# Optimization experiments

Hardware: AMD Instinct MI355X
Metric: run time of the kernel (lower is better)

## Reference

```python
import jax, jax.numpy as jnp
import numpy as np

B, D, S, F, C, H, OUT = 4, 60, 512, 158, 64, 128, 1
LN_EPS = 1e-5


def setup_inputs() -> dict:
    key = jax.random.key(0)
    ks = jax.random.split(key, 12)
    g = lambda k, shape, s=0.05: jax.random.normal(k, shape, dtype=jnp.float32) * s
    return dict(
        x=jax.random.normal(ks[0], (B, D, S, F), dtype=jnp.float32),
        feature_mask=jax.random.randint(ks[1], (B, D, S), 0, 2).astype(bool),
        wq=g(ks[2], (F, C)), bq=jnp.zeros((C,), jnp.float32),
        wk=g(ks[3], (F, C)), bk=jnp.zeros((C,), jnp.float32),
        wv=g(ks[4], (F, C)), bv=jnp.zeros((C,), jnp.float32),
        ln_g=jnp.ones((F + C,), jnp.float32), ln_b=jnp.zeros((F + C,), jnp.float32),
        w_ih=g(ks[5], (3 * H, F + C)), w_hh=g(ks[6], (3 * H, H)),
        b_ih=jnp.zeros((3 * H,), jnp.float32), b_hh=jnp.zeros((3 * H,), jnp.float32),
        w1=g(ks[7], (H, H // 2)), b1=jnp.zeros((H // 2,), jnp.float32),
        w2=g(ks[8], (H // 2, OUT)), b2=jnp.zeros((OUT,), jnp.float32),
    )


def reference(x, feature_mask, wq, bq, wk, bk, wv, bv, ln_g, ln_b,
              w_ih, w_hh, b_ih, b_hh, w1, b1, w2, b2):
    b, d, s, f = x.shape
    c = wq.shape[1]
    h_dim = w_hh.shape[1]

    # --- market context attention, vectorized over (batch, days) ---
    Q = x @ wq + bq            # (B,D,S,C)
    K = x @ wk + bk
    V = x @ wv + bv
    scores = jnp.einsum('bdsc,bdtc->bdst', Q, K) / jnp.sqrt(jnp.float32(c))
    scores = jnp.where(feature_mask[:, :, None, :], scores, -1e9)  # mask keys
    attn = jax.nn.softmax(scores, axis=-1)
    ctx = jnp.einsum('bdst,bdtc->bdsc', attn, V)       # (B,D,S,C)
    ctx = jnp.where(feature_mask[..., None], ctx, 0.0)  # mask queries
    denom = jnp.maximum(feature_mask.sum(axis=2), 1).astype(x.dtype)  # (B,D)
    market = ctx.sum(axis=2) / denom[..., None]         # (B,D,C)

    # --- concat + layernorm ---
    aug = jnp.concatenate(
        [x, jnp.broadcast_to(market[:, :, None, :], (b, d, s, c))], axis=-1)
    mu = aug.mean(-1, keepdims=True)
    var = aug.var(-1, keepdims=True)
    aug = (aug - mu) / jnp.sqrt(var + LN_EPS) * ln_g + ln_b  # (B,D,S,F+C)

    # --- GRU over days, batch = B*S independent sequences ---
    seq = aug.transpose(1, 0, 2, 3).reshape(d, b * s, f + c)  # (D, N, F+C)
    x_proj = seq @ w_ih.T + b_ih                               # (D, N, 3H)

    def step(h, xp):
        hp = h @ w_hh.T + b_hh
        xr, xz, xn = jnp.split(xp, 3, axis=-1)
        hr, hz, hn = jnp.split(hp, 3, axis=-1)
        r = jax.nn.sigmoid(xr + hr)
        z = jax.nn.sigmoid(xz + hz)
        n = jnp.tanh(xn + r * hn)
        return (1.0 - z) * n + z * h, None

    h0 = jnp.zeros((b * s, h_dim), x.dtype)
    h_last, _ = jax.lax.scan(step, h0, x_proj)  # last-step output
    h_last = h_last.reshape(b, s, h_dim)

    # --- output head (dropout inactive in eval) ---
    hid = jax.nn.relu(h_last @ w1 + b1)
    return hid @ w2 + b2  # (B, S, OUT)
```

## Files before the change

### kernel.cpp

```cpp
#include <hip/hip_runtime.h>
#include <hip/hip_bf16.h>
#include <math.h>

#define BB 4
#define DD 60
#define SS 512
#define FF 158
#define CC 64
#define HH 128
#define FC 222
#define G3 384
#define NN 2048
#define BDN 240

#define L2E  1.44269504f
#define L2E2 2.88539008f
#define QSCALE 0.18033688f

typedef _Float16 f16x8 __attribute__((ext_vector_type(8)));
typedef _Float16 f16x4 __attribute__((ext_vector_type(4)));
typedef float f32x4 __attribute__((ext_vector_type(4)));

__device__ __forceinline__ float exp2_hw(float x){ return __builtin_amdgcn_exp2f(x); }
__device__ __forceinline__ float rcp_hw(float x){ return __builtin_amdgcn_rcpf(x); }

__global__ void prep_kernel(const float* __restrict__ w_ih,
                            const float* __restrict__ wq, const float* __restrict__ wk,
                            const float* __restrict__ w_hh,
                            _Float16* __restrict__ wf16, _Float16* __restrict__ wqk,
                            _Float16* __restrict__ whh16){
    int idx = blockIdx.x*256 + threadIdx.x;
    if (idx < 384*224){
        int n = idx / 224, k = idx % 224;
        float sc = (n < 256) ? L2E : L2E2;
        wf16[idx] = (k < FC) ? (_Float16)(w_ih[n*FC + k] * sc) : (_Float16)0.0f;
    } else if (idx < 384*224 + 128*160){
        int i2 = idx - 384*224;
        int n = i2 / 160, k = i2 % 160;
        float v = 0.0f;
        if (k < FF)
            v = (n < 64) ? wq[k*CC + n] : wk[k*CC + (n-64)];
        wqk[i2] = (_Float16)v;
    } else {
        int i3 = idx - (384*224 + 128*160);
        if (i3 < 384*128){
            int n = i3 / 128;
            float sc = (n < 256) ? L2E : L2E2;
            whh16[i3] = (_Float16)(w_hh[i3] * sc);
        }
    }
}

__global__ __launch_bounds__(256) void qk_kernel(const float* __restrict__ x,
                           const _Float16* __restrict__ wqk,
                           const float* __restrict__ bq, const float* __restrict__ bk,
                           _Float16* __restrict__ Qh, _Float16* __restrict__ Kh){
    __shared__ _Float16 xa[5][64][40];
    int tid  = threadIdx.x;
    int lane = tid & 63, wv = tid >> 6;
    int col  = lane & 15, quad = lane >> 4;
    int row0 = blockIdx.x * 64;

    f16x8 bfr[2][5];
    #pragma unroll
    for (int nt = 0; nt < 2; ++nt){
        int n = wv*32 + nt*16 + col;
        #pragma unroll
        for (int kq = 0; kq < 5; ++kq)
            bfr[nt][kq] = *(const f16x8*)&wqk[n*160 + kq*32 + quad*8];
    }

    if (tid < 128){
        int r = tid >> 1;
        xa[4][r][30 + (tid & 1)] = (_Float16)0.0f;
    }
    {
        const float4* xb4 = (const float4*)(x + (size_t)row0*FF);
        #pragma unroll
        for (int j = 0; j < 10; ++j){
            int i = tid + j*256;
            if (i < 2528){
                float4 v = xb4[i];
                int base = i*4;
                #pragma unroll
                for (int e = 0; e < 4; ++e){
                    int idx = base + e;
                    int r = idx / 158;
                    int k = idx - r*158;
                    xa[k >> 5][r][k & 31] = (_Float16)((&v.x)[e]);
                }
            }
        }
    }
    __syncthreads();

    float bias[2];
    #pragma unroll
    for (int nt = 0; nt < 2; ++nt){
        int n = wv*32 + nt*16 + col;
        bias[nt] = (n < 64) ? bq[n] : bk[n-64];
    }

    #pragma unroll 1
    for (int mt = 0; mt < 4; ++mt){
        f16x8 a[5];
        #pragma unroll
        for (int kq = 0; kq < 5; ++kq)
            a[kq] = *(const f16x8*)&xa[kq][mt*16 + col][quad*8];
        #pragma unroll
        for (int nt = 0; nt < 2; ++nt){
            f32x4 c = {0.0f, 0.0f, 0.0f, 0.0f};
            #pragma unroll
            for (int kq = 0; kq < 5; ++kq)
                c = __builtin_amdgcn_mfma_f32_16x16x32_f16(a[kq], bfr[nt][kq], c, 0, 0, 0);
            int n = wv*32 + nt*16 + col;
            #pragma unroll
            for (int reg = 0; reg < 4; ++reg){
                int row = row0 + mt*16 + quad*4 + reg;
                float val = c[reg] + bias[nt];
                if (n < 64) Qh[(size_t)row*CC + n]      = (_Float16)(val * QSCALE);
                else        Kh[(size_t)row*CC + (n-64)] = (_Float16)val;
            }
        }
    }
}

__global__ __launch_bounds__(512) void attn_kernel(const _Float16* __restrict__ Qh,
                                                   const _Float16* __restrict__ Kh,
                                                   const int* __restrict__ mask,
                                                   const float* __restrict__ x,
                                                   const float* __restrict__ wv,
                                                   const float* __restrict__ bv,
                                                   float* __restrict__ market){
    __shared__ _Float16 kf[2][512][32];
    __shared__ float w_sh[512];
    __shared__ float mk_lds[512];

    int tid  = threadIdx.x;
    int bd   = blockIdx.x;
    int lane = tid & 63, wvw = tid >> 6;
    int col  = lane & 15, quad = lane >> 4;

    const _Float16* qb = Qh + (size_t)(bd*SS)*CC;
    const _Float16* kb = Kh + (size_t)(bd*SS)*CC;

    {
        int t = tid;
        w_sh[t] = 0.0f;
        mk_lds[t] = (mask[bd*SS + t] != 0) ? 1.0f : 0.0f;
    }
    for (int i = tid; i < 4096; i += 512){
        int t = i >> 3, ch = i & 7;
        *(f16x8*)&kf[ch >> 2][t][(ch & 3)*8] = *(const f16x8*)&kb[t*CC + ch*8];
    }

    f16x8 a0[4], a1[4];
    #pragma unroll
    for (int af = 0; af < 4; ++af){
        int row = wvw*64 + af*16 + col;
        a0[af] = *(const f16x8*)&qb[row*CC + quad*8];
        a1[af] = *(const f16x8*)&qb[row*CC + 32 + quad*8];
    }
    __syncthreads();

    float lacc[4][4] = {{0,0,0,0},{0,0,0,0},{0,0,0,0},{0,0,0,0}};
    #pragma unroll 2
    for (int kt = 0; kt < 32; ++kt){
        f16x8 b0 = *(const f16x8*)&kf[0][kt*16 + col][quad*8];
        f16x8 b1 = *(const f16x8*)&kf[1][kt*16 + col][quad*8];
        float mkv = mk_lds[kt*16 + col];
        #pragma unroll
        for (int af = 0; af < 4; ++af){
            f32x4 c = {0.0f, 0.0f, 0.0f, 0.0f};
            c = __builtin_amdgcn_mfma_f32_16x16x32_f16(a0[af], b0, c, 0, 0, 0);
            c = __builtin_amdgcn_mfma_f32_16x16x32_f16(a1[af], b1, c, 0, 0, 0);
            #pragma unroll
            for (int reg = 0; reg < 4; ++reg)
                lacc[af][reg] += exp2_hw(c[reg]) * mkv;
        }
    }
    float crv[4][4];
    #pragma unroll
    for (int af = 0; af < 4; ++af){
        #pragma unroll
        for (int reg = 0; reg < 4; ++reg){
            float l = lacc[af][reg];
            l += __shfl_xor(l, 1, 64);
            l += __shfl_xor(l, 2, 64);
            l += __shfl_xor(l, 4, 64);
            l += __shfl_xor(l, 8, 64);
            int row = wvw*64 + af*16 + quad*4 + reg;
            crv[af][reg] = mk_lds[row] * rcp_hw(l);
        }
    }

    #pragma unroll 2
    for (int kt = 0; kt < 32; ++kt){
        f16x8 b0 = *(const f16x8*)&kf[0][kt*16 + col][quad*8];
        f16x8 b1 = *(const f16x8*)&kf[1][kt*16 + col][quad*8];
        float s = 0.0f;
        #pragma unroll
        for (int af = 0; af < 4; ++af){
            f32x4 c = {0.0f, 0.0f, 0.0f, 0.0f};
            c = __builtin_amdgcn_mfma_f32_16x16x32_f16(a0[af], b0, c, 0, 0, 0);
            c = __builtin_amdgcn_mfma_f32_16x16x32_f16(a1[af], b1, c, 0, 0, 0);
            #pragma unroll
            for (int reg = 0; reg < 4; ++reg)
                s = fmaf(exp2_hw(c[reg]), crv[af][reg], s);
        }
        s += __shfl_xor(s, 16, 64);
        s += __shfl_xor(s, 32, 64);
        if (quad == 0)
            atomicAdd(&w_sh[kt*16 + col], s);
    }
    __syncthreads();

    w_sh[tid] *= mk_lds[tid];
    __syncthreads();

    float* part = (float*)kf;
    {
        int tg = tid >> 8;
        int kk = tid & 255;
        float acc = 0.0f;
        if (kk < FF){
            const float* xb = x + ((size_t)bd*SS + tg*256)*FF + kk;
            #pragma unroll 8
            for (int t = 0; t < 256; ++t)
                acc = fmaf(w_sh[tg*256 + t], xb[(size_t)t*FF], acc);
        }
        part[tg*256 + kk] = acc;
    }
    __syncthreads();
    if (tid < 64){
        int c = tid;
        float m = 0.0f;
        for (int k = 0; k < FF; ++k){
            float y = part[k] + part[256 + k];
            m = fmaf(y, wv[k*CC + c], m);
        }
        float cnt = 0.0f, sw = 0.0f;
        #pragma unroll
        for (int j = 0; j < 8; ++j){
            cnt += mk_lds[c + 64*j];
            sw  += w_sh[c + 64*j];
        }
        #pragma unroll
        for (int o = 1; o < 64; o <<= 1){
            cnt += __shfl_xor(cnt, o, 64);
            sw  += __shfl_xor(sw,  o, 64);
        }
        market[bd*CC + c] = (m + sw*bv[c]) * rcp_hw(fmaxf(cnt, 1.0f));
    }
}

__global__ __launch_bounds__(512, 2) void xproj_kernel(const float* __restrict__ x,
                             const float* __restrict__ market,
                             const float* __restrict__ ln_g, const float* __restrict__ ln_b,
                             const _Float16* __restrict__ wf16, const float* __restrict__ b_ih,
                             _Float16* __restrict__ XPP){
    __shared__ _Float16 aug[7][64][32];
    int tid  = threadIdx.x;
    int lane = tid & 63, wv = tid >> 6;
    int col  = lane & 15, quad = lane >> 4;
    int row0 = blockIdx.x * 64;

    f16x8 bfr[3][7];
    #pragma unroll
    for (int nt = 0; nt < 3; ++nt){
        int n = wv*48 + nt*16 + col;
        #pragma unroll
        for (int kq = 0; kq < 7; ++kq)
            bfr[nt][kq] = *(const f16x8*)&wf16[n*224 + kq*32 + quad*8];
    }

    {
        int wrow = wv*8 + (lane >> 3);
        int g    = lane & 7;
        int row  = row0 + wrow;
        int d = row / NN, n = row % NN;
        int b = n >> 9, s = n & 511;
        const float* xr = &x[((size_t)((b*DD + d)*SS) + s)*FF];
        const float* mr = &market[(b*DD + d)*CC];
        float v[28];
        float sum = 0.0f, sq = 0.0f;
        #pragma unroll
        for (int j = 0; j < 28; ++j){
            int f = g + 8*j;
            float vv = 0.0f;
            if (f < FF) vv = xr[f];
            else if (f < FC) vv = mr[f - FF];
            v[j] = vv;
            sum += vv; sq += vv*vv;
        }
        sum += __shfl_xor(sum,1,64); sq += __shfl_xor(sq,1,64);
        sum += __shfl_xor(sum,2,64); sq += __shfl_xor(sq,2,64);
        sum += __shfl_xor(sum,4,64); sq += __shfl_xor(sq,4,64);
        float mu   = sum * (1.0f/222.0f);
        float var  = sq * (1.0f/222.0f) - mu*mu;
        float rstd = rsqrtf(var + 1e-5f);
        #pragma unroll
        for (int j = 0; j < 28; ++j){
            int f = g + 8*j;
            float val = (f < FC) ? ((v[j]-mu)*rstd*ln_g[f] + ln_b[f]) : 0.0f;
            aug[f>>5][wrow][f&31] = (_Float16)val;
        }
    }
    __syncthreads();

    float bias[3];
    #pragma unroll
    for (int nt = 0; nt < 3; ++nt){
        int n = wv*48 + nt*16 + col;
        bias[nt] = b_ih[n] * ((n < 256) ? L2E : L2E2);
    }
    const int d    = row0 / NN;
    const int blk0 = (row0 % NN) >> 4;
    #pragma unroll 1
    for (int mt = 0; mt < 4; ++mt){
        f16x8 a[7];
        #pragma unroll
        for (int kq = 0; kq < 7; ++kq)
            a[kq] = *(const f16x8*)&aug[kq][mt*16 + col][quad*8];
        _Float16* obase = XPP + ((size_t)(d*128 + blk0 + mt)*G3) * 16 + quad*4;
        #pragma unroll
        for (int nt = 0; nt < 3; ++nt){
            f32x4 c = {0.0f, 0.0f, 0.0f, 0.0f};
            #pragma unroll
            for (int kq = 0; kq < 7; ++kq)
                c = __builtin_amdgcn_mfma_f32_16x16x32_f16(a[kq], bfr[nt][kq], c, 0, 0, 0);
            int nn = wv*48 + nt*16 + col;
            f16x4 pk;
            pk[0] = (_Float16)(c[0] + bias[nt]);
            pk[1] = (_Float16)(c[1] + bias[nt]);
            pk[2] = (_Float16)(c[2] + bias[nt]);
            pk[3] = (_Float16)(c[3] + bias[nt]);
            *(f16x4*)(obase + (size_t)nn*16) = pk;
        }
    }
}

#define XLOAD(dst, base_) do{                                                   \
    dst[0][0] = *(const f16x4*)((base_));                                       \
    dst[0][1] = *(const f16x4*)((base_) + 128*16);                              \
    dst[0][2] = *(const f16x4*)((base_) + 256*16);                              \
    dst[1][0] = *(const f16x4*)((base_) + 16*16);                               \
    dst[1][1] = *(const f16x4*)((base_) + 144*16);                              \
    dst[1][2] = *(const f16x4*)((base_) + 272*16);                              \
}while(0)

#define BARRIER_NODRAIN() asm volatile("s_waitcnt lgkmcnt(0)\ns_barrier" ::: "memory")

#define GRU_STEP(PRD, PWR, XC, XPF, DOPF) do{                                   \
    if (DOPF) { XLOAD(XPF, xp_d + 2*DSTR); }                                    \
    f16x8 a_[4];                                                                \
    _Pragma("unroll") for (int kq = 0; kq < 4; ++kq)                            \
        a_[kq] = *(const f16x8*)&hfrag[PRD][kq][col][quad*8];                   \
    f32x4 c_[3][2];                                                             \
    _Pragma("unroll") for (int g = 0; g < 3; ++g)                               \
    _Pragma("unroll") for (int hf = 0; hf < 2; ++hf){                           \
        f32x4 acc = {0.0f, 0.0f, 0.0f, 0.0f};                                   \
        _Pragma("unroll") for (int kq = 0; kq < 4; ++kq)                        \
            acc = __builtin_amdgcn_mfma_f32_16x16x32_f16(a_[kq], bfr[g][hf][kq], acc, 0,0,0); \
        c_[g][hf] = acc;                                                        \
    }                                                                           \
    _Pragma("unroll") for (int hf = 0; hf < 2; ++hf)                            \
    _Pragma("unroll") for (int rg = 0; rg < 4; ++rg){                           \
        float r_ = rcp_hw(1.0f + exp2_hw(-((float)XC[hf][0][rg] + c_[0][hf][rg] + bh[0][hf]))); \
        float z_ = rcp_hw(1.0f + exp2_hw(-((float)XC[hf][1][rg] + c_[1][hf][rg] + bh[1][hf]))); \
        float e_ = exp2_hw((float)XC[hf][2][rg] + r_*(c_[2][hf][rg] + bh[2][hf])); \
        float n_ = 1.0f - 2.0f*rcp_hw(e_ + 1.0f);                               \
        float h_ = n_ + z_*(hcur[hf][rg] - n_);                                 \
        hcur[hf][rg] = h_;                                                      \
        hfrag[PWR][w][quad*4 + rg][hf*16 + col] = (_Float16)h_;                 \
    }                                                                           \
    xp_d += DSTR;                                                               \
    BARRIER_NODRAIN();                                                          \
}while(0)

__global__ __launch_bounds__(256, 1) void gru_kernel(const _Float16* __restrict__ XPP,
                                                     const _Float16* __restrict__ whh16,
                                                     const float* __restrict__ b_hh,
                                                     const float* __restrict__ w1, const float* __restrict__ b1,
                                                     const float* __restrict__ w2, const float* __restrict__ b2,
                                                     float* __restrict__ out){
    __shared__ _Float16 hfrag[2][4][16][40];
    __shared__ float h_sh[16][132];

    const int tid  = threadIdx.x;
    const int lane = tid & 63, w = tid >> 6;
    const int col  = lane & 15, quad = lane >> 4;
    const int row0 = blockIdx.x * 16;

    for (int i = tid; i < 2*4*16*40; i += 256)
        ((_Float16*)hfrag)[i] = (_Float16)0.0f;

    f16x8 bfr[3][2][4];
    #pragma unroll
    for (int g = 0; g < 3; ++g)
    #pragma unroll
    for (int hf = 0; hf < 2; ++hf){
        int n = g*HH + w*32 + hf*16 + col;
        #pragma unroll
        for (int kq = 0; kq < 4; ++kq)
            bfr[g][hf][kq] = *(const f16x8*)&whh16[(size_t)n*HH + kq*32 + quad*8];
    }

    float bh[3][2];
    #pragma unroll
    for (int g = 0; g < 3; ++g)
    #pragma unroll
    for (int hf = 0; hf < 2; ++hf)
        bh[g][hf] = b_hh[g*HH + w*32 + hf*16 + col] * ((g < 2) ? L2E : L2E2);

    const size_t DSTR = (size_t)128 * G3 * 16;
    const _Float16* xp_d = XPP + ((size_t)blockIdx.x*G3 + (w*32 + col))*16 + quad*4;

    f16x4 xA[2][3], xB[2][3], xC[2][3];
    XLOAD(xA, xp_d);
    XLOAD(xB, xp_d + DSTR);

    float hcur[2][4] = {{0,0,0,0},{0,0,0,0}};
    __syncthreads();

    #pragma unroll 1
    for (int ch = 0; ch < 10; ++ch){
        const int pf = (ch < 9);
        GRU_STEP(0, 1, xA, xC, 1);
        GRU_STEP(1, 0, xB, xA, 1);
        GRU_STEP(0, 1, xC, xB, 1);
        GRU_STEP(1, 0, xA, xC, 1);
        GRU_STEP(0, 1, xB, xA, pf);
        GRU_STEP(1, 0, xC, xB, pf);
    }

    #pragma unroll
    for (int hf = 0; hf < 2; ++hf)
    #pragma unroll
    for (int rg = 0; rg < 4; ++rg)
        h_sh[quad*4 + rg][w*32 + hf*16 + col] = hcur[hf][rg];
    __syncthreads();

    {
        int c2 = tid & 63;
        int rb = tid >> 6;
        #pragma unroll
        for (int rr = 0; rr < 4; ++rr){
            int r = rb*4 + rr;
            float acc = 0.0f;
            #pragma unroll 8
            for (int k = 0; k < 128; ++k)
                acc = fmaf(h_sh[r][k], w1[k*64 + c2], acc);
            float hid = fmaxf(acc + b1[c2], 0.0f);
            float o = hid * w2[c2];
            #pragma unroll
            for (int off = 1; off < 64; off <<= 1) o += __shfl_xor(o, off, 64);
            if (c2 == 0) out[row0 + r] = o + b2[0];
        }
    }
}

extern "C" void kernel_launch(void* const* d_in, const int* in_sizes, int n_in,
                              void* d_out, int out_size, void* d_ws, size_t ws_size,
                              hipStream_t stream) {
    const float* x    = (const float*)d_in[0];
    const int*   mask = (const int*)d_in[1];
    const float* wq   = (const float*)d_in[2];
    const float* bq   = (const float*)d_in[3];
    const float* wk   = (const float*)d_in[4];
    const float* bk   = (const float*)d_in[5];
    const float* wv   = (const float*)d_in[6];
    const float* bv   = (const float*)d_in[7];
    const float* ln_g = (const float*)d_in[8];
    const float* ln_b = (const float*)d_in[9];
    const float* w_ih = (const float*)d_in[10];
    const float* w_hh = (const float*)d_in[11];
    const float* b_ih = (const float*)d_in[12];
    const float* b_hh = (const float*)d_in[13];
    const float* w1   = (const float*)d_in[14];
    const float* b1   = (const float*)d_in[15];
    const float* w2   = (const float*)d_in[16];
    const float* b2   = (const float*)d_in[17];

    float* ws = (float*)d_ws;
    _Float16* Qh  = (_Float16*)ws;
    _Float16* Kh  = (_Float16*)(ws + 3932160);
    _Float16* XPP = (_Float16*)ws;
    float* market = ws + 23592960;
    _Float16* wf16 = (_Float16*)(ws + 23608320);
    _Float16* wqk  = (_Float16*)(ws + 23651328);
    _Float16* whh16= (_Float16*)(ws + 23666688);

    prep_kernel<<<648, 256, 0, stream>>>(w_ih, wq, wk, w_hh, wf16, wqk, whh16);
    qk_kernel<<<1920, 256, 0, stream>>>(x, wqk, bq, bk, Qh, Kh);
    attn_kernel<<<240, 512, 0, stream>>>(Qh, Kh, mask, x, wv, bv, market);
    xproj_kernel<<<1920, 512, 0, stream>>>(x, market, ln_g, ln_b, wf16, b_ih, XPP);
    gru_kernel<<<128, 256, 0, stream>>>(XPP, whh16, b_hh, w1, b1, w2, b2, (float*)d_out);
}
```

Before: 343.4 us.

## Split attention and GRU work across twice as many blocks to fill more CUs

The attention kernel now runs two blocks per (batch, day), each handling half of the query rows. The blocks accumulate key weights into a global buffer with atomics, and that buffer is zeroed in the prep kernel. The market-vector reduction moves into a new market_kernel. The GRU kernel launches 256 blocks of 8 sequences each instead of 128 blocks of 16, with half the lanes idle in the gate math, so more CUs run the serial recurrence. The cost is an extra kernel launch, global atomics, and wasted MFMA rows in the GRU.

```diff
diff --git a/kernel.cpp b/kernel.cpp
--- a/kernel.cpp
+++ b/kernel.cpp
@@ -28,8 +28,9 @@
                             const float* __restrict__ wq, const float* __restrict__ wk,
                             const float* __restrict__ w_hh,
                             _Float16* __restrict__ wf16, _Float16* __restrict__ wqk,
-                            _Float16* __restrict__ whh16){
+                            _Float16* __restrict__ whh16, float* __restrict__ Wg){
     int idx = blockIdx.x*256 + threadIdx.x;
+    if (idx < BDN*SS) Wg[idx] = 0.0f;
     if (idx < 384*224){
         int n = idx / 224, k = idx % 224;
         float sc = (n < 256) ? L2E : L2E2;
@@ -128,16 +129,14 @@
 __global__ __launch_bounds__(512) void attn_kernel(const _Float16* __restrict__ Qh,
                                                    const _Float16* __restrict__ Kh,
                                                    const int* __restrict__ mask,
-                                                   const float* __restrict__ x,
-                                                   const float* __restrict__ wv,
-                                                   const float* __restrict__ bv,
-                                                   float* __restrict__ market){
+                                                   float* __restrict__ Wg){
     __shared__ _Float16 kf[2][512][32];
     __shared__ float w_sh[512];
     __shared__ float mk_lds[512];
 
     int tid  = threadIdx.x;
-    int bd   = blockIdx.x;
+    int bd   = blockIdx.x >> 1;
+    int q0   = (blockIdx.x & 1) * 256;
     int lane = tid & 63, wvw = tid >> 6;
     int col  = lane & 15, quad = lane >> 4;
 
@@ -154,23 +153,23 @@
         *(f16x8*)&kf[ch >> 2][t][(ch & 3)*8] = *(const f16x8*)&kb[t*CC + ch*8];
     }
 
-    f16x8 a0[4], a1[4];
-    #pragma unroll
-    for (int af = 0; af < 4; ++af){
-        int row = wvw*64 + af*16 + col;
+    f16x8 a0[2], a1[2];
+    #pragma unroll
+    for (int af = 0; af < 2; ++af){
+        int row = q0 + wvw*32 + af*16 + col;
         a0[af] = *(const f16x8*)&qb[row*CC + quad*8];
         a1[af] = *(const f16x8*)&qb[row*CC + 32 + quad*8];
     }
     __syncthreads();
 
-    float lacc[4][4] = {{0,0,0,0},{0,0,0,0},{0,0,0,0},{0,0,0,0}};
+    float lacc[2][4] = {{0,0,0,0},{0,0,0,0}};
     #pragma unroll 2
     for (int kt = 0; kt < 32; ++kt){
         f16x8 b0 = *(const f16x8*)&kf[0][kt*16 + col][quad*8];
         f16x8 b1 = *(const f16x8*)&kf[1][kt*16 + col][quad*8];
         float mkv = mk_lds[kt*16 + col];
         #pragma unroll
-        for (int af = 0; af < 4; ++af){
+        for (int af = 0; af < 2; ++af){
             f32x4 c = {0.0f, 0.0f, 0.0f, 0.0f};
             c = __builtin_amdgcn_mfma_f32_16x16x32_f16(a0[af], b0, c, 0, 0, 0);
             c = __builtin_amdgcn_mfma_f32_16x16x32_f16(a1[af], b1, c, 0, 0, 0);
@@ -179,9 +178,9 @@
                 lacc[af][reg] += exp2_hw(c[reg]) * mkv;
         }
     }
-    float crv[4][4];
-    #pragma unroll
-    for (int af = 0; af < 4; ++af){
+    float crv[2][4];
+    #pragma unroll
+    for (int af = 0; af < 2; ++af){
         #pragma unroll
         for (int reg = 0; reg < 4; ++reg){
             float l = lacc[af][reg];
@@ -189,7 +188,7 @@
             l += __shfl_xor(l, 2, 64);
             l += __shfl_xor(l, 4, 64);
             l += __shfl_xor(l, 8, 64);
-            int row = wvw*64 + af*16 + quad*4 + reg;
+            int row = q0 + wvw*32 + af*16 + quad*4 + reg;
             crv[af][reg] = mk_lds[row] * rcp_hw(l);
         }
     }
@@ -200,7 +199,7 @@
         f16x8 b1 = *(const f16x8*)&kf[1][kt*16 + col][quad*8];
         float s = 0.0f;
         #pragma unroll
-        for (int af = 0; af < 4; ++af){
+        for (int af = 0; af < 2; ++af){
             f32x4 c = {0.0f, 0.0f, 0.0f, 0.0f};
             c = __builtin_amdgcn_mfma_f32_16x16x32_f16(a0[af], b0, c, 0, 0, 0);
             c = __builtin_amdgcn_mfma_f32_16x16x32_f16(a1[af], b1, c, 0, 0, 0);
@@ -215,10 +214,27 @@
     }
     __syncthreads();
 
-    w_sh[tid] *= mk_lds[tid];
-    __syncthreads();
-
-    float* part = (float*)kf;
+    atomicAdd(&Wg[bd*SS + tid], w_sh[tid]);
+}
+
+__global__ __launch_bounds__(512) void market_kernel(const float* __restrict__ Wg,
+                                                     const int* __restrict__ mask,
+                                                     const float* __restrict__ x,
+                                                     const float* __restrict__ wv,
+                                                     const float* __restrict__ bv,
+                                                     float* __restrict__ market){
+    __shared__ float wt[512];
+    __shared__ float mk[512];
+    __shared__ float part[512];
+
+    int tid = threadIdx.x;
+    int bd  = blockIdx.x;
+
+    float m_ = (mask[bd*SS + tid] != 0) ? 1.0f : 0.0f;
+    mk[tid] = m_;
+    wt[tid] = Wg[bd*SS + tid] * m_;
+    __syncthreads();
+
     {
         int tg = tid >> 8;
         int kk = tid & 255;
@@ -227,7 +243,7 @@
             const float* xb = x + ((size_t)bd*SS + tg*256)*FF + kk;
             #pragma unroll 8
             for (int t = 0; t < 256; ++t)
-                acc = fmaf(w_sh[tg*256 + t], xb[(size_t)t*FF], acc);
+                acc = fmaf(wt[tg*256 + t], xb[(size_t)t*FF], acc);
         }
         part[tg*256 + kk] = acc;
     }
@@ -242,8 +258,8 @@
         float cnt = 0.0f, sw = 0.0f;
         #pragma unroll
         for (int j = 0; j < 8; ++j){
-            cnt += mk_lds[c + 64*j];
-            sw  += w_sh[c + 64*j];
+            cnt += mk[c + 64*j];
+            sw  += wt[c + 64*j];
         }
         #pragma unroll
         for (int o = 1; o < 64; o <<= 1){
@@ -352,7 +368,7 @@
 #define BARRIER_NODRAIN() asm volatile("s_waitcnt lgkmcnt(0)\ns_barrier" ::: "memory")
 
 #define GRU_STEP(PRD, PWR, XC, XPF, DOPF) do{                                   \
-    if (DOPF) { XLOAD(XPF, xp_d + 2*DSTR); }                                    \
+    if (DOPF && qlow) { XLOAD(XPF, xp_d + 2*DSTR); }                            \
     f16x8 a_[4];                                                                \
     _Pragma("unroll") for (int kq = 0; kq < 4; ++kq)                            \
         a_[kq] = *(const f16x8*)&hfrag[PRD][kq][col][quad*8];                   \
@@ -364,6 +380,7 @@
             acc = __builtin_amdgcn_mfma_f32_16x16x32_f16(a_[kq], bfr[g][hf][kq], acc, 0,0,0); \
         c_[g][hf] = acc;                                                        \
     }                                                                           \
+    if (qlow){                                                                  \
     _Pragma("unroll") for (int hf = 0; hf < 2; ++hf)                            \
     _Pragma("unroll") for (int rg = 0; rg < 4; ++rg){                           \
         float r_ = rcp_hw(1.0f + exp2_hw(-((float)XC[hf][0][rg] + c_[0][hf][rg] + bh[0][hf]))); \
@@ -373,24 +390,25 @@
         float h_ = n_ + z_*(hcur[hf][rg] - n_);                                 \
         hcur[hf][rg] = h_;                                                      \
         hfrag[PWR][w][quad*4 + rg][hf*16 + col] = (_Float16)h_;                 \
-    }                                                                           \
+    }}                                                                          \
     xp_d += DSTR;                                                               \
     BARRIER_NODRAIN();                                                          \
 }while(0)
 
-__global__ __launch_bounds__(256, 1) void gru_kernel(const _Float16* __restrict__ XPP,
+__global__ __launch_bounds__(256, 2) void gru_kernel(const _Float16* __restrict__ XPP,
                                                      const _Float16* __restrict__ whh16,
                                                      const float* __restrict__ b_hh,
                                                      const float* __restrict__ w1, const float* __restrict__ b1,
                                                      const float* __restrict__ w2, const float* __restrict__ b2,
                                                      float* __restrict__ out){
     __shared__ _Float16 hfrag[2][4][16][40];
-    __shared__ float h_sh[16][132];
+    __shared__ float h_sh[8][132];
 
     const int tid  = threadIdx.x;
     const int lane = tid & 63, w = tid >> 6;
     const int col  = lane & 15, quad = lane >> 4;
-    const int row0 = blockIdx.x * 16;
+    const bool qlow = (quad < 2);
+    const int row0 = blockIdx.x * 8;
 
     for (int i = tid; i < 2*4*16*40; i += 256)
         ((_Float16*)hfrag)[i] = (_Float16)0.0f;
@@ -414,11 +432,14 @@
         bh[g][hf] = b_hh[g*HH + w*32 + hf*16 + col] * ((g < 2) ? L2E : L2E2);
 
     const size_t DSTR = (size_t)128 * G3 * 16;
-    const _Float16* xp_d = XPP + ((size_t)blockIdx.x*G3 + (w*32 + col))*16 + quad*4;
+    const _Float16* xp_d = XPP + ((size_t)(blockIdx.x >> 1)*G3 + (w*32 + col))*16
+                               + (blockIdx.x & 1)*8 + quad*4;
 
     f16x4 xA[2][3], xB[2][3], xC[2][3];
-    XLOAD(xA, xp_d);
-    XLOAD(xB, xp_d + DSTR);
+    if (qlow){
+        XLOAD(xA, xp_d);
+        XLOAD(xB, xp_d + DSTR);
+    }
 
     float hcur[2][4] = {{0,0,0,0},{0,0,0,0}};
     __syncthreads();
@@ -434,19 +455,21 @@
         GRU_STEP(1, 0, xC, xB, pf);
     }
 
-    #pragma unroll
-    for (int hf = 0; hf < 2; ++hf)
-    #pragma unroll
-    for (int rg = 0; rg < 4; ++rg)
-        h_sh[quad*4 + rg][w*32 + hf*16 + col] = hcur[hf][rg];
+    if (qlow){
+        #pragma unroll
+        for (int hf = 0; hf < 2; ++hf)
+        #pragma unroll
+        for (int rg = 0; rg < 4; ++rg)
+            h_sh[quad*4 + rg][w*32 + hf*16 + col] = hcur[hf][rg];
+    }
     __syncthreads();
 
     {
         int c2 = tid & 63;
         int rb = tid >> 6;
         #pragma unroll
-        for (int rr = 0; rr < 4; ++rr){
-            int r = rb*4 + rr;
+        for (int rr = 0; rr < 2; ++rr){
+            int r = rb + rr*4;
             float acc = 0.0f;
             #pragma unroll 8
             for (int k = 0; k < 128; ++k)
@@ -485,15 +508,17 @@
     float* ws = (float*)d_ws;
     _Float16* Qh  = (_Float16*)ws;
     _Float16* Kh  = (_Float16*)(ws + 3932160);
+    float*    Wg  = ws + 8000000;
     _Float16* XPP = (_Float16*)ws;
     float* market = ws + 23592960;
     _Float16* wf16 = (_Float16*)(ws + 23608320);
     _Float16* wqk  = (_Float16*)(ws + 23651328);
     _Float16* whh16= (_Float16*)(ws + 23666688);
 
-    prep_kernel<<<648, 256, 0, stream>>>(w_ih, wq, wk, w_hh, wf16, wqk, whh16);
+    prep_kernel<<<648, 256, 0, stream>>>(w_ih, wq, wk, w_hh, wf16, wqk, whh16, Wg);
     qk_kernel<<<1920, 256, 0, stream>>>(x, wqk, bq, bk, Qh, Kh);
-    attn_kernel<<<240, 512, 0, stream>>>(Qh, Kh, mask, x, wv, bv, market);
+    attn_kernel<<<480, 512, 0, stream>>>(Qh, Kh, mask, Wg);
+    market_kernel<<<240, 512, 0, stream>>>(Wg, mask, x, wv, bv, market);
     xproj_kernel<<<1920, 512, 0, stream>>>(x, market, ln_g, ln_b, wf16, b_ih, XPP);
-    gru_kernel<<<128, 256, 0, stream>>>(XPP, whh16, b_hh, w1, b1, w2, b2, (float*)d_out);
-}
+    gru_kernel<<<256, 256, 0, stream>>>(XPP, whh16, b_hh, w1, b1, w2, b2, (float*)d_out);
+}
```

Measured after the change: 349.2 us. No clear change (+1.7%).
